# Kernel tuning notes

Hardware: AMD Instinct MI355X
Metric: run time of the kernel (lower is better)

## Reference

```python
import jax, jax.numpy as jnp
import numpy as np

B, S, D = 4, 8192, 512
H, DK = 8, 64
LOCAL_W = 256
GLOBAL_STRIDE = 64
LN_EPS = 1e-5


def setup_inputs() -> dict:
    key = jax.random.key(0)
    ks = jax.random.split(key, 9)
    scale = 1.0 / np.sqrt(D)
    def lin(k, din, dout):
        return jax.random.normal(k, (din, dout), jnp.float32) * scale
    return {
        "x": jax.random.normal(ks[0], (B, S, D), jnp.float32),
        "lq_w": lin(ks[1], D, D), "lq_b": jnp.zeros((D,), jnp.float32),
        "lk_w": lin(ks[2], D, D), "lk_b": jnp.zeros((D,), jnp.float32),
        "lv_w": lin(ks[3], D, D), "lv_b": jnp.zeros((D,), jnp.float32),
        "gq_w": lin(ks[4], D, D), "gq_b": jnp.zeros((D,), jnp.float32),
        "gk_w": lin(ks[5], D, D), "gk_b": jnp.zeros((D,), jnp.float32),
        "gv_w": lin(ks[6], D, D), "gv_b": jnp.zeros((D,), jnp.float32),
        "out_w": jax.random.normal(ks[7], (2 * D, D), jnp.float32) * (1.0 / np.sqrt(2 * D)),
        "out_b": jnp.zeros((D,), jnp.float32),
        "ln_g": jnp.ones((D,), jnp.float32),
        "ln_b": jnp.zeros((D,), jnp.float32),
    }


def _local_attention(x, qw, qb, kw, kb, vw, vb):
    # x: [B,S,D]; S divisible by LOCAL_W -> no padding path.
    nW = S // LOCAL_W
    xw = x.reshape(B, nW, LOCAL_W, D)
    def heads(w, b):
        y = jnp.einsum('bnwd,de->bnwe', xw, w) + b  # [B,nW,W,D]
        return y.reshape(B, nW, LOCAL_W, H, DK).transpose(0, 1, 3, 2, 4)  # [B,nW,H,W,dk]
    q, k, v = heads(qw, qb), heads(kw, kb), heads(vw, vb)
    scores = jnp.einsum('bnhqd,bnhkd->bnhqk', q, k) / np.sqrt(DK)
    attn = jax.nn.softmax(scores, axis=-1)
    out = jnp.einsum('bnhqk,bnhkd->bnhqd', attn, v)  # [B,nW,H,W,dk]
    return out.transpose(0, 1, 3, 2, 4).reshape(B, S, D)


def _global_attention(x, qw, qb, kw, kb, vw, vb):
    gc = x[:, ::GLOBAL_STRIDE]                       # [B,G,D]
    G = gc.shape[1]
    q = (x @ qw + qb).reshape(B, S, H, DK)           # [B,S,H,dk]
    k = (gc @ kw + kb).reshape(B, G, H, DK)
    v = (gc @ vw + vb).reshape(B, G, H, DK)
    scores = jnp.einsum('bshd,bghd->bhsg', q, k) / np.sqrt(DK)
    attn = jax.nn.softmax(scores, axis=-1)
    out = jnp.einsum('bhsg,bghd->bshd', attn, v)
    return out.reshape(B, S, D)


def reference(x, lq_w, lq_b, lk_w, lk_b, lv_w, lv_b,
              gq_w, gq_b, gk_w, gk_b, gv_w, gv_b,
              out_w, out_b, ln_g, ln_b):
    local = _local_attention(x, lq_w, lq_b, lk_w, lk_b, lv_w, lv_b)
    glob = _global_attention(x, gq_w, gq_b, gk_w, gk_b, gv_w, gv_b)
    combined = jnp.concatenate([local, glob], axis=-1) @ out_w + out_b
    h = x + combined  # dropout is identity in eval
    mu = jnp.mean(h, axis=-1, keepdims=True)
    var = jnp.var(h, axis=-1, keepdims=True)
    return (h - mu) / jnp.sqrt(var + LN_EPS) * ln_g + ln_b
```

## Files before the change

### kernel.cpp

```cpp
#include <hip/hip_runtime.h>
#include <hip/hip_bf16.h>
#include <stdint.h>

#define B_ 4
#define S_ 8192
#define D_ 512
#define H_ 8
#define DK_ 64
#define G_ 128
#define ROWS_ (B_*S_)

typedef unsigned short u16;
typedef __attribute__((ext_vector_type(8))) short short8;
typedef __attribute__((ext_vector_type(4))) short short4v;
typedef __attribute__((ext_vector_type(4))) float floatx4;

static __device__ __forceinline__ float bf2f(u16 u){
  union { uint32_t i; float f; } v; v.i = ((uint32_t)u) << 16; return v.f;
}
static __device__ __forceinline__ u16 f2bf(float f){
  union { float f; uint32_t i; } v; v.f = f;
  uint32_t u = v.i; u += 0x7fff + ((u >> 16) & 1); return (u16)(u >> 16);
}

static __device__ __forceinline__ void glds16(const u16* g, u16* l){
  __builtin_amdgcn_global_load_lds(
      (const __attribute__((address_space(1))) void*)g,
      (__attribute__((address_space(3))) void*)l, 16, 0, 0);
}

__global__ void cast_x_kernel(const float* __restrict__ x, u16* __restrict__ xb,
                              u16* __restrict__ xg, int n4){
  int i = blockIdx.x*blockDim.x + threadIdx.x;
  if (i >= n4) return;
  float4 v = ((const float4*)x)[i];
  short4v o;
  o[0] = (short)f2bf(v.x); o[1] = (short)f2bf(v.y);
  o[2] = (short)f2bf(v.z); o[3] = (short)f2bf(v.w);
  *(short4v*)(xb + (size_t)i*4) = o;
  int row = i >> 7;
  if ((row & 63) == 0){
    int b = row >> 13, g = (row & 8191) >> 6;
    *(short4v*)(xg + ((size_t)(b*G_ + g)*D_) + (i & 127)*4) = o;
  }
}

__global__ void transpose_cast_kernel(const float* __restrict__ W, u16* __restrict__ Ot, int K, int N){
  __shared__ float t[64][65];
  int n0 = blockIdx.x*64, k0 = blockIdx.y*64;
  int tx = threadIdx.x & 63, ty = threadIdx.x >> 6;
#pragma unroll
  for (int j=0;j<16;j++){ int k = ty + j*4; t[k][tx] = W[(size_t)(k0+k)*N + n0+tx]; }
  __syncthreads();
#pragma unroll
  for (int j=0;j<16;j++){ int n = ty + j*4; Ot[(size_t)(n0+n)*K + k0 + tx] = f2bf(t[tx][n]); }
}

__global__ void transpose_cast6_kernel(const float* s0, const float* s1, const float* s2,
    const float* s3, const float* s4, const float* s5,
    u16* __restrict__ WcatT, u16* __restrict__ WgT){
  __shared__ float t[64][65];
  int z = blockIdx.z;
  const float* W = (z==0)?s0:(z==1)?s1:(z==2)?s2:(z==3)?s3:(z==4)?s4:s5;
  u16* Ot = (z<4) ? (WcatT + (size_t)z*512*512) : (WgT + (size_t)(z-4)*512*512);
  int n0 = blockIdx.x*64, k0 = blockIdx.y*64;
  int tx = threadIdx.x & 63, ty = threadIdx.x >> 6;
#pragma unroll
  for (int j=0;j<16;j++){ int k = ty + j*4; t[k][tx] = W[(size_t)(k0+k)*512 + n0+tx]; }
  __syncthreads();
#pragma unroll
  for (int j=0;j<16;j++){ int n = ty + j*4; Ot[(size_t)(n0+n)*512 + k0 + tx] = f2bf(t[tx][n]); }
}

__global__ void build_bias_kernel(float* __restrict__ bcat, float* __restrict__ bg,
    const float* lq_b, const float* lk_b, const float* lv_b, const float* gq_b,
    const float* gk_b, const float* gv_b){
  int i = blockIdx.x*blockDim.x + threadIdx.x;
  if (i < 2048){
    const float* s = (i < 512) ? lq_b : (i < 1024) ? lk_b : (i < 1536) ? lv_b : gq_b;
    bcat[i] = s[i & 511];
  } else if (i < 3072){
    int j = i - 2048;
    bg[j] = (j < 512) ? gk_b[j] : gv_b[j - 512];
  }
}

template<int EPI>
__global__ __launch_bounds__(512, 1) void gemm_big(
    const u16* __restrict__ A, const u16* __restrict__ Bt,
    const float* __restrict__ bias, u16* __restrict__ C,
    const u16* __restrict__ X, int M, int N, int K)
{
  __shared__ u16 SM[4][16384];
  const int tid = threadIdx.x, lane = tid & 63, w = tid >> 6;
  const int wm = w >> 2, wn = w & 3;
  const int gx = gridDim.x;
  const int h = blockIdx.y * gx + blockIdx.x;
  const int chunk = (gx * gridDim.y) >> 3;
  const int work = (h & 7) * chunk + (h >> 3);
  const int bx = work % gx, by = work / gx;
  const int m0 = by*256, n0 = bx*256;
  const int T = K >> 5;

  const u16* gsrc[4]; int loff[4];
#pragma unroll
  for (int j = 0; j < 4; j++){
    int fb  = w*4 + j;
    int isB = fb >> 4;
    int blk = fb & 15;
    const u16* bp = isB ? Bt : A;
    int row = (isB ? n0 : m0) + blk*16 + (lane & 15);
    gsrc[j] = bp + (size_t)row * K + ((lane >> 4) * 8);
    loff[j] = fb*512;
  }

  floatx4 acc[8][4] = {};

  auto stageT = [&](int tt){
    u16* Sb_ = &SM[tt & 3][0];
#pragma unroll
    for (int j = 0; j < 4; j++) glds16(gsrc[j] + tt*32, Sb_ + loff[j]);
  };
  auto readFrags = [&](short8* Sa, short8* Sb, int slot){
    const u16* Tb = &SM[slot][0];
#pragma unroll
    for (int i=0;i<8;i++) Sa[i] = *(const short8*)(Tb + (wm*8 + i)*512 + lane*8);
#pragma unroll
    for (int j=0;j<4;j++) Sb[j] = *(const short8*)(Tb + (16 + wn*4 + j)*512 + lane*8);
  };
  auto doMfma = [&](const short8* Sa, const short8* Sb){
#pragma unroll
    for (int i=0;i<8;i++)
#pragma unroll
      for (int j=0;j<4;j++)
        acc[i][j] = __builtin_amdgcn_mfma_f32_16x16x32_bf16(Sa[i], Sb[j], acc[i][j], 0,0,0);
  };

  short8 A0[8], B0[4], A1[8], B1[4];

  stageT(0); stageT(1); stageT(2);
  asm volatile("s_waitcnt vmcnt(8)" ::: "memory");
  __builtin_amdgcn_s_barrier();
  readFrags(A0, B0, 0);

  for (int t = 0; t < T; t += 2){
    if (t + 2 < T) asm volatile("s_waitcnt vmcnt(4)" ::: "memory");
    else           asm volatile("s_waitcnt vmcnt(0)" ::: "memory");
    __builtin_amdgcn_s_barrier();
    if (t + 3 < T) stageT(t + 3);
    readFrags(A1, B1, (t + 1) & 3);
    doMfma(A0, B0);

    if (t + 3 < T) asm volatile("s_waitcnt vmcnt(4)" ::: "memory");
    else           asm volatile("s_waitcnt vmcnt(0)" ::: "memory");
    __builtin_amdgcn_s_barrier();
    if (t + 4 < T) stageT(t + 4);
    if (t + 2 < T) readFrags(A0, B0, (t + 2) & 3);
    doMfma(A1, B1);
  }

#pragma unroll
  for (int mi=0; mi<8; mi++)
#pragma unroll
    for (int nj=0; nj<4; nj++){
      int col = n0 + (wn*4 + nj)*16 + (lane & 15);
      float bv = bias[col];
#pragma unroll
      for (int ii=0; ii<4; ii++){
        size_t row = (size_t)(m0 + (wm*8 + mi)*16 + (lane>>4)*4 + ii);
        float v = acc[mi][nj][ii] + bv;
        if (EPI == 1) v += bf2f(X[row*N + col]);
        C[row*N + col] = f2bf(v);
      }
    }
}

__global__ __launch_bounds__(256) void gemm_small(
    const u16* __restrict__ A, const u16* __restrict__ Bt,
    const float* __restrict__ bias, u16* __restrict__ C,
    int M, int N, int K)
{
  __shared__ u16 As[128*32];
  __shared__ u16 Bs[128*32];
  const int tid = threadIdx.x, lane = tid & 63, w = tid >> 6;
  const int m0 = blockIdx.y*128, n0 = blockIdx.x*128;
  const int wm = (w>>1)*64, wn = (w&1)*64;
  floatx4 acc[4][4] = {};
  const int c0 = 2*w;
  const int sr = lane >> 2;
  const int sc = (lane & 3) * 8;
  const u16* ga0 = A  + (size_t)(m0 +  c0     *16 + sr)*K + sc;
  const u16* ga1 = A  + (size_t)(m0 + (c0 + 1)*16 + sr)*K + sc;
  const u16* gb0 = Bt + (size_t)(n0 +  c0     *16 + sr)*K + sc;
  const u16* gb1 = Bt + (size_t)(n0 + (c0 + 1)*16 + sr)*K + sc;
  u16* la0 = &As[ c0     *512];
  u16* la1 = &As[(c0 + 1)*512];
  u16* lb0 = &Bs[ c0     *512];
  u16* lb1 = &Bs[(c0 + 1)*512];

  for (int k0 = 0; k0 < K; k0 += 32){
    __syncthreads();
    glds16(ga0 + k0, la0);
    glds16(ga1 + k0, la1);
    glds16(gb0 + k0, lb0);
    glds16(gb1 + k0, lb1);
    __syncthreads();
    short8 af[4], bf[4];
#pragma unroll
    for (int i=0;i<4;i++) af[i] = *(const short8*)&As[(wm + i*16 + (lane&15))*32 + (lane>>4)*8];
#pragma unroll
    for (int i=0;i<4;i++) bf[i] = *(const short8*)&Bs[(wn + i*16 + (lane&15))*32 + (lane>>4)*8];
#pragma unroll
    for (int mi=0;mi<4;mi++)
#pragma unroll
      for (int ni=0;ni<4;ni++)
        acc[mi][ni] = __builtin_amdgcn_mfma_f32_16x16x32_bf16(af[mi], bf[ni], acc[mi][ni], 0,0,0);
  }

#pragma unroll
  for (int mi=0;mi<4;mi++)
#pragma unroll
    for (int ni=0;ni<4;ni++){
      int col = n0 + wn + ni*16 + (lane&15);
      float bv = bias[col];
#pragma unroll
      for (int i=0;i<4;i++){
        size_t row = (size_t)(m0 + wm + mi*16 + (lane>>4)*4 + i);
        C[row*N + col] = f2bf(acc[mi][ni][i] + bv);
      }
    }
}

template<int KVLEN, int KSTRIDE, bool GLOBAL>
__global__ __launch_bounds__(512, 2) void attn_kernel(
    const u16* __restrict__ qkv, const u16* __restrict__ kvbuf, u16* __restrict__ comb)
{
  __shared__ u16 SM[KVLEN*256];
  u16* Kl = SM;
  u16* Vt = SM + KVLEN*64;
  u16* Pl = SM + KVLEN*128;
  const int tid = threadIdx.x, lane = tid & 63, w = tid >> 6;
  const int h = blockIdx.x, n = blockIdx.y, b = blockIdx.z;
  const size_t qrow0 = (size_t)b*S_ + (size_t)n*256;
  const int krow0 = GLOBAL ? b*G_ : (b*S_ + n*256);
  const int qc = (GLOBAL ? 1536 : 0)   + h*DK_;
  const int kc = (GLOBAL ? 0    : 512) + h*DK_;
  const int vc = (GLOBAL ? 512  : 1024)+ h*DK_;
  const int oc = (GLOBAL ? 512  : 0)   + h*DK_;
  constexpr int NF = KVLEN/16;

  {
    const int rpw = KVLEN/8;
    const int r0w = w * rpw;
    const int cg = ((lane & 7) ^ (lane >> 3)) * 8;
    const int rl = lane >> 3;
#pragma unroll
    for (int j = 0; j < rpw; j += 8){
      int row = r0w + j + rl;
      glds16(kvbuf + (size_t)(krow0 + row)*KSTRIDE + kc + cg, &Kl[(r0w + j)*64]);
    }
  }
  if (tid < (KVLEN/4)*8){
    const int rb = tid >> 3;
    const int kv0 = rb * 4;
    const int d0 = (tid & 7) * 8;
    const u16* vp = kvbuf + (size_t)(krow0 + kv0)*KSTRIDE + vc + d0;
    short8 rIn[4];
#pragma unroll
    for (int i=0;i<4;i++) rIn[i] = *(const short8*)(vp + (size_t)i*KSTRIDE);
    const int c   = rb >> 1;
    const int sub = kv0 & 7;
#pragma unroll
    for (int dd=0; dd<8; dd++){
      int d = d0 + dd;
      short4v o;
#pragma unroll
      for (int j=0;j<4;j++) o[j] = rIn[j][dd];
      *(short4v*)&Vt[d*KVLEN + ((c ^ (d&7)) << 3) + sub] = o;
    }
  }
  __syncthreads();

  const float sc2 = 0.125f * 1.44269504f;
  const int Pbase = w*16*KVLEN;

  for (int sp = 2*w; sp < 2*w + 2; sp++){
    const u16* qp = qkv + (qrow0 + sp*16 + (lane&15))*2048 + qc + ((lane>>4)*8);
    short8 qf0 = *(const short8*)qp;
    short8 qf1 = *(const short8*)(qp + 32);

    floatx4 sacc[NF];
#pragma unroll
    for (int nf = 0; nf < NF; nf++){
      const u16* kb = &Kl[(nf*16 + (lane&15))*64];
      short8 kf0 = *(const short8*)(kb + ((( lane>>4)      ^ (lane&7)) << 3));
      short8 kf1 = *(const short8*)(kb + ((((lane>>4) + 4) ^ (lane&7)) << 3));
      floatx4 z = {0.f,0.f,0.f,0.f};
      z = __builtin_amdgcn_mfma_f32_16x16x32_bf16(qf0, kf0, z, 0,0,0);
      z = __builtin_amdgcn_mfma_f32_16x16x32_bf16(qf1, kf1, z, 0,0,0);
      sacc[nf] = z;
    }

    float sm[4] = {0.f,0.f,0.f,0.f};
#pragma unroll
    for (int nf=0;nf<NF;nf++)
#pragma unroll
      for (int i=0;i<4;i++){
        float e = exp2f(sacc[nf][i] * sc2);
        sacc[nf][i] = e; sm[i] += e;
      }
#pragma unroll
    for (int i=0;i<4;i++){
#pragma unroll
      for (int msk=1; msk<16; msk<<=1) sm[i] += __shfl_xor(sm[i], msk);
      sm[i] = 1.f / sm[i];
    }

#pragma unroll
    for (int nf=0;nf<NF;nf++)
#pragma unroll
      for (int i=0;i<4;i++){
        int row = (lane>>4)*4 + i;
        int ch  = nf*2 + ((lane>>3)&1);
        Pl[Pbase + row*KVLEN + ((ch ^ (row&7)) << 3) + (lane&7)] = f2bf(sacc[nf][i]*sm[i]);
      }

    floatx4 oacc[4] = {};
#pragma unroll
    for (int kk=0; kk<KVLEN/32; kk++){
      int prow = lane & 15;
      short8 pf = *(const short8*)&Pl[Pbase + prow*KVLEN + (((kk*4 + (lane>>4)) ^ (prow&7)) << 3)];
#pragma unroll
      for (int nd=0; nd<4; nd++){
        int d = nd*16 + (lane&15);
        short8 vf = *(const short8*)&Vt[d*KVLEN + (((kk*4 + (lane>>4)) ^ (d&7)) << 3)];
        oacc[nd] = __builtin_amdgcn_mfma_f32_16x16x32_bf16(pf, vf, oacc[nd], 0,0,0);
      }
    }

#pragma unroll
    for (int nd=0; nd<4; nd++)
#pragma unroll
      for (int i=0;i<4;i++){
        size_t row = qrow0 + sp*16 + (lane>>4)*4 + i;
        comb[row*1024 + oc + nd*16 + (lane&15)] = f2bf(oacc[nd][i]);
      }
  }
}

__global__ __launch_bounds__(256) void ln_kernel(const u16* __restrict__ hb,
    float* __restrict__ out, const float* __restrict__ g, const float* __restrict__ bta){
  int lane = threadIdx.x & 63, w = threadIdx.x >> 6;
  size_t row = (size_t)blockIdx.x*4 + w;
  const u16* p = hb + row*D_;
  short8 hv = *(const short8*)(p + lane*8);
  float f[8]; float s = 0.f, q = 0.f;
#pragma unroll
  for (int i=0;i<8;i++){ f[i] = bf2f((u16)hv[i]); s += f[i]; q += f[i]*f[i]; }
#pragma unroll
  for (int msk=1; msk<64; msk<<=1){ s += __shfl_xor(s, msk); q += __shfl_xor(q, msk); }
  float mean = s * (1.f/512.f);
  float var  = q * (1.f/512.f) - mean*mean;
  float inv  = rsqrtf(var + 1e-5f);
  float4 g0 = ((const float4*)g)[lane*2],   g1 = ((const float4*)g)[lane*2+1];
  float4 b0 = ((const float4*)bta)[lane*2], b1 = ((const float4*)bta)[lane*2+1];
  float4 o0, o1;
  o0.x = (f[0]-mean)*inv*g0.x + b0.x; o0.y = (f[1]-mean)*inv*g0.y + b0.y;
  o0.z = (f[2]-mean)*inv*g0.z + b0.z; o0.w = (f[3]-mean)*inv*g0.w + b0.w;
  o1.x = (f[4]-mean)*inv*g1.x + b1.x; o1.y = (f[5]-mean)*inv*g1.y + b1.y;
  o1.z = (f[6]-mean)*inv*g1.z + b1.z; o1.w = (f[7]-mean)*inv*g1.w + b1.w;
  float* op = out + row*D_;
  ((float4*)op)[lane*2]     = o0;
  ((float4*)op)[lane*2 + 1] = o1;
}

extern "C" void kernel_launch(void* const* d_in, const int* in_sizes, int n_in,
                              void* d_out, int out_size, void* d_ws, size_t ws_size,
                              hipStream_t stream)
{
  const float* x    = (const float*)d_in[0];
  const float* lq_w = (const float*)d_in[1];
  const float* lq_b = (const float*)d_in[2];
  const float* lk_w = (const float*)d_in[3];
  const float* lk_b = (const float*)d_in[4];
  const float* lv_w = (const float*)d_in[5];
  const float* lv_b = (const float*)d_in[6];
  const float* gq_w = (const float*)d_in[7];
  const float* gq_b = (const float*)d_in[8];
  const float* gk_w = (const float*)d_in[9];
  const float* gk_b = (const float*)d_in[10];
  const float* gv_w = (const float*)d_in[11];
  const float* gv_b = (const float*)d_in[12];
  const float* out_w = (const float*)d_in[13];
  const float* out_b = (const float*)d_in[14];
  const float* ln_g = (const float*)d_in[15];
  const float* ln_b = (const float*)d_in[16];

  char* ws = (char*)d_ws;
  size_t off = 0;
  auto alloc = [&](size_t bytes)->void*{ void* p = ws + off; off += (bytes + 255) & ~255ULL; return p; };
  u16*  xb    = (u16*) alloc((size_t)ROWS_*D_*2);
  u16*  xg    = (u16*) alloc((size_t)512*512*2);
  u16*  WcatT = (u16*) alloc((size_t)2048*512*2);
  u16*  WgT   = (u16*) alloc((size_t)1024*512*2);
  u16*  WoutT = (u16*) alloc((size_t)512*1024*2);
  float* bcat = (float*)alloc(2048*4);
  float* bg   = (float*)alloc(1024*4);
  u16*  qkvg  = (u16*) alloc((size_t)ROWS_*2048*2);
  u16*  gkv   = (u16*) alloc((size_t)512*1024*2);
  u16*  comb  = (u16*) alloc((size_t)ROWS_*1024*2);
  u16*  hbuf  = qkvg;

  cast_x_kernel<<<16384,256,0,stream>>>(x, xb, xg, ROWS_*D_/4);
  transpose_cast6_kernel<<<dim3(8,8,6),256,0,stream>>>(lq_w, lk_w, lv_w, gq_w, gk_w, gv_w, WcatT, WgT);
  transpose_cast_kernel<<<dim3(8,16),256,0,stream>>>(out_w, WoutT, 1024, 512);
  build_bias_kernel<<<12,256,0,stream>>>(bcat, bg, lq_b, lk_b, lv_b, gq_b, gk_b, gv_b);

  gemm_big<0><<<dim3(8,128),512,0,stream>>>(xb, WcatT, bcat, qkvg, nullptr, ROWS_, 2048, 512);
  gemm_small<<<dim3(8,4),256,0,stream>>>(xg, WgT, bg, gkv, 512, 1024, 512);

  attn_kernel<256,2048,false><<<dim3(8,32,4),512,0,stream>>>(qkvg, qkvg, comb);
  attn_kernel<128,1024,true ><<<dim3(8,32,4),512,0,stream>>>(qkvg, gkv,  comb);

  gemm_big<1><<<dim3(2,128),512,0,stream>>>(comb, WoutT, out_b, hbuf, xb,
      ROWS_, 512, 1024);
  ln_kernel<<<8192,256,0,stream>>>(hbuf, (float*)d_out, ln_g, ln_b);
}
```

Baseline: 277.0 us.

## Chunk attention over 64-key blocks to shrink P buffer and raise occupancy

Restructures the attention kernel to process keys in chunks of 64. Each chunk computes scores, exponentiates them, writes unnormalized P to a small per-wave LDS tile and immediately accumulates P·V. Normalization by the row sum is deferred to the output write. This cuts the P scratch in LDS from KVLEN*128 to 8192 elements and reduces live score registers, which allows 4 blocks per CU instead of 2. It relies on no max-subtraction, as before, and stores unnormalized exponentials in bf16. The P tile is reused across chunks without a barrier, which is safe only because each wave owns its own tile.

New measurement: 263.0 us, median of 3. 1.05x faster.

```diff
diff --git a/kernel.cpp b/kernel.cpp
--- a/kernel.cpp
+++ b/kernel.cpp
@@ -232,10 +232,10 @@
 }
 
 template<int KVLEN, int KSTRIDE, bool GLOBAL>
-__global__ __launch_bounds__(512, 2) void attn_kernel(
+__global__ __launch_bounds__(512, 4) void attn_kernel(
     const u16* __restrict__ qkv, const u16* __restrict__ kvbuf, u16* __restrict__ comb)
 {
-  __shared__ u16 SM[KVLEN*256];
+  __shared__ u16 SM[KVLEN*128 + 8192];
   u16* Kl = SM;
   u16* Vt = SM + KVLEN*64;
   u16* Pl = SM + KVLEN*128;
@@ -247,7 +247,7 @@
   const int kc = (GLOBAL ? 0    : 512) + h*DK_;
   const int vc = (GLOBAL ? 512  : 1024)+ h*DK_;
   const int oc = (GLOBAL ? 512  : 0)   + h*DK_;
-  constexpr int NF = KVLEN/16;
+  constexpr int NC = KVLEN/64;
 
   {
     const int rpw = KVLEN/8;
@@ -282,68 +282,64 @@
   __syncthreads();
 
   const float sc2 = 0.125f * 1.44269504f;
-  const int Pbase = w*16*KVLEN;
+  const int Pbase = w*16*64;
 
   for (int sp = 2*w; sp < 2*w + 2; sp++){
     const u16* qp = qkv + (qrow0 + sp*16 + (lane&15))*2048 + qc + ((lane>>4)*8);
     short8 qf0 = *(const short8*)qp;
     short8 qf1 = *(const short8*)(qp + 32);
 
-    floatx4 sacc[NF];
-#pragma unroll
-    for (int nf = 0; nf < NF; nf++){
-      const u16* kb = &Kl[(nf*16 + (lane&15))*64];
-      short8 kf0 = *(const short8*)(kb + ((( lane>>4)      ^ (lane&7)) << 3));
-      short8 kf1 = *(const short8*)(kb + ((((lane>>4) + 4) ^ (lane&7)) << 3));
-      floatx4 z = {0.f,0.f,0.f,0.f};
-      z = __builtin_amdgcn_mfma_f32_16x16x32_bf16(qf0, kf0, z, 0,0,0);
-      z = __builtin_amdgcn_mfma_f32_16x16x32_bf16(qf1, kf1, z, 0,0,0);
-      sacc[nf] = z;
-    }
-
+    floatx4 oacc[4] = {};
     float sm[4] = {0.f,0.f,0.f,0.f};
-#pragma unroll
-    for (int nf=0;nf<NF;nf++)
-#pragma unroll
-      for (int i=0;i<4;i++){
-        float e = exp2f(sacc[nf][i] * sc2);
-        sacc[nf][i] = e; sm[i] += e;
+
+#pragma unroll
+    for (int c = 0; c < NC; c++){
+      floatx4 sacc[4];
+#pragma unroll
+      for (int nf = 0; nf < 4; nf++){
+        const u16* kb = &Kl[((c*4 + nf)*16 + (lane&15))*64];
+        short8 kf0 = *(const short8*)(kb + ((( lane>>4)      ^ (lane&7)) << 3));
+        short8 kf1 = *(const short8*)(kb + ((((lane>>4) + 4) ^ (lane&7)) << 3));
+        floatx4 z = {0.f,0.f,0.f,0.f};
+        z = __builtin_amdgcn_mfma_f32_16x16x32_bf16(qf0, kf0, z, 0,0,0);
+        z = __builtin_amdgcn_mfma_f32_16x16x32_bf16(qf1, kf1, z, 0,0,0);
+        sacc[nf] = z;
       }
+#pragma unroll
+      for (int nf=0;nf<4;nf++)
+#pragma unroll
+        for (int i=0;i<4;i++){
+          float e = exp2f(sacc[nf][i] * sc2);
+          sm[i] += e;
+          int row = (lane>>4)*4 + i;
+          int ch  = nf*2 + ((lane>>3)&1);
+          Pl[Pbase + row*64 + ((ch ^ (row&7)) << 3) + (lane&7)] = f2bf(e);
+        }
+#pragma unroll
+      for (int kk=0; kk<2; kk++){
+        int prow = lane & 15;
+        short8 pf = *(const short8*)&Pl[Pbase + prow*64 + (((kk*4 + (lane>>4)) ^ (prow&7)) << 3)];
+#pragma unroll
+        for (int nd=0; nd<4; nd++){
+          int d = nd*16 + (lane&15);
+          short8 vf = *(const short8*)&Vt[d*KVLEN + (((c*8 + kk*4 + (lane>>4)) ^ (d&7)) << 3)];
+          oacc[nd] = __builtin_amdgcn_mfma_f32_16x16x32_bf16(pf, vf, oacc[nd], 0,0,0);
+        }
+      }
+    }
+
 #pragma unroll
     for (int i=0;i<4;i++){
 #pragma unroll
       for (int msk=1; msk<16; msk<<=1) sm[i] += __shfl_xor(sm[i], msk);
       sm[i] = 1.f / sm[i];
     }
-
-#pragma unroll
-    for (int nf=0;nf<NF;nf++)
-#pragma unroll
-      for (int i=0;i<4;i++){
-        int row = (lane>>4)*4 + i;
-        int ch  = nf*2 + ((lane>>3)&1);
-        Pl[Pbase + row*KVLEN + ((ch ^ (row&7)) << 3) + (lane&7)] = f2bf(sacc[nf][i]*sm[i]);
-      }
-
-    floatx4 oacc[4] = {};
-#pragma unroll
-    for (int kk=0; kk<KVLEN/32; kk++){
-      int prow = lane & 15;
-      short8 pf = *(const short8*)&Pl[Pbase + prow*KVLEN + (((kk*4 + (lane>>4)) ^ (prow&7)) << 3)];
-#pragma unroll
-      for (int nd=0; nd<4; nd++){
-        int d = nd*16 + (lane&15);
-        short8 vf = *(const short8*)&Vt[d*KVLEN + (((kk*4 + (lane>>4)) ^ (d&7)) << 3)];
-        oacc[nd] = __builtin_amdgcn_mfma_f32_16x16x32_bf16(pf, vf, oacc[nd], 0,0,0);
-      }
-    }
-
 #pragma unroll
     for (int nd=0; nd<4; nd++)
 #pragma unroll
       for (int i=0;i<4;i++){
         size_t row = qrow0 + sp*16 + (lane>>4)*4 + i;
-        comb[row*1024 + oc + nd*16 + (lane&15)] = f2bf(oacc[nd][i]);
+        comb[row*1024 + oc + nd*16 + (lane&15)] = f2bf(oacc[nd][i] * sm[i]);
       }
   }
 }
```
